# Kernel tuning notes

Measured on AMD Instinct MI355X. Metric: run time of the kernel, lower is better.

## Reference

```python
import jax, jax.numpy as jnp
import numpy as np

B, S, H, D = 2, 2048, 16, 64
DM = H * D  # 1024


def setup_inputs() -> dict:
    key = jax.random.key(0)
    ks = jax.random.split(key, 5)
    scale = 0.02
    return {
        "hidden_states": jax.random.normal(ks[0], (B, S, DM), dtype=jnp.float32),
        "Wq": scale * jax.random.normal(ks[1], (DM, DM), dtype=jnp.float32),
        "bq": jnp.zeros((DM,), jnp.float32),
        "Wk": scale * jax.random.normal(ks[2], (DM, DM), dtype=jnp.float32),
        "bk": jnp.zeros((DM,), jnp.float32),
        "Wv": scale * jax.random.normal(ks[3], (DM, DM), dtype=jnp.float32),
        "bv": jnp.zeros((DM,), jnp.float32),
        "Wy": scale * jax.random.normal(ks[4], (DM, DM), dtype=jnp.float32),
        "by": jnp.zeros((DM,), jnp.float32),
    }


def _split_heads(x):
    # [B,S,H*D] -> [B,H,S,D]
    b, s, _ = x.shape
    return x.reshape(b, s, H, D).transpose(0, 2, 1, 3)


def _merge_heads(x):
    # [B,H,S,D] -> [B,S,H*D]
    b, h, s, d = x.shape
    return x.transpose(0, 2, 1, 3).reshape(b, s, h * d)


def reference(hidden_states, Wq, bq, Wk, bk, Wv, bv, Wy, by):
    q = _split_heads(hidden_states @ Wq.T + bq)  # [B,H,S,D]
    k = _split_heads(hidden_states @ Wk.T + bk)
    v = _split_heads(hidden_states @ Wv.T + bv)

    logits = jnp.einsum("bhsd,bhtd->bhst", q, k) / jnp.sqrt(jnp.float32(D))
    mask = jnp.tril(jnp.ones((S, S), jnp.float32))  # causal lower-triangular mask

    # Faithful to the original module's hand-rolled masked softmax:
    # denominator = sum_t exp(logits) * mask ; numerator = exp(logits*mask - 1e4*(1-mask))
    denom = jnp.sum(jnp.exp(logits) * mask, axis=3, keepdims=True)
    numer = jnp.exp(logits * mask - 1e4 * (1.0 - mask))
    weights = numer / denom  # [B,H,S,S]

    attended = jnp.einsum("bhst,bhtd->bhsd", weights, v)
    out = _merge_heads(attended)  # [B,S,H*D]
    return out @ Wy.T + by
```

## Files before the change

### kernel.cpp

```cpp
#include <hip/hip_runtime.h>

#define DEV __device__ __forceinline__

typedef __attribute__((ext_vector_type(8))) short bf16x8;
typedef __attribute__((ext_vector_type(4))) float f32x4;
typedef __attribute__((ext_vector_type(16))) float f32x16;

DEV ushort f2bf(float f) {
  union { float f; unsigned u; } x; x.f = f;
  unsigned r = (x.u + 0x7FFFu + ((x.u >> 16) & 1u)) >> 16;
  return (ushort)r;
}

DEV void gload16(const void* g, void* l) {
  __builtin_amdgcn_global_load_lds(
      (const __attribute__((address_space(1))) void*)g,
      (__attribute__((address_space(3))) void*)l, 16, 0, 0);
}

DEV f32x4 mfma16(bf16x8 a, bf16x8 b, f32x4 c) {
  return __builtin_amdgcn_mfma_f32_16x16x32_bf16(a, b, c, 0, 0, 0);
}
DEV f32x16 mfma32(bf16x8 a, bf16x8 b, f32x16 c) {
  return __builtin_amdgcn_mfma_f32_32x32x16_bf16(a, b, c, 0, 0, 0);
}

DEV unsigned cvtpk(float a, float b) {
  unsigned r;
  asm("v_cvt_pk_bf16_f32 %0, %1, %2" : "=v"(r) : "v"(a), "v"(b));
  return r;
}

#if __has_builtin(__builtin_amdgcn_exp2f)
#define EXP2(x) __builtin_amdgcn_exp2f(x)
#else
#define EXP2(x) exp2f(x)
#endif

#define BB 2
#define SS 2048
#define HH 16
#define DD 64
#define DM 1024
#define MROWS (BB * SS)
#define NQKV  (3 * DM)

__global__ void convert_kernel(const float* __restrict__ hs,
                               const float* __restrict__ Wq, const float* __restrict__ bq,
                               const float* __restrict__ Wk, const float* __restrict__ bk,
                               const float* __restrict__ Wv, const float* __restrict__ bv,
                               const float* __restrict__ Wy,
                               ushort* __restrict__ Xb, ushort* __restrict__ Wqkv,
                               ushort* __restrict__ Wyb, float* __restrict__ bqkv) {
  const int HS_V = (MROWS * DM) / 4;
  const int WQ_V = (NQKV * DM) / 4;
  const int WY_V = (DM * DM) / 4;
  int idx = blockIdx.x * 256 + threadIdx.x;
  if (idx < HS_V) {
    float4 v = ((const float4*)hs)[idx];
    ushort4 o; o.x = f2bf(v.x); o.y = f2bf(v.y); o.z = f2bf(v.z); o.w = f2bf(v.w);
    ((ushort4*)Xb)[idx] = o;
  } else if (idx < HS_V + WQ_V) {
    int e = (idx - HS_V) * 4;
    int n = e >> 10, k = e & 1023;
    const float* W = (n < 1024) ? Wq : (n < 2048) ? Wk : Wv;
    int nn = n & 1023;
    float4 v = *(const float4*)(W + nn * 1024 + k);
    ushort4 o; o.x = f2bf(v.x); o.y = f2bf(v.y); o.z = f2bf(v.z); o.w = f2bf(v.w);
    ((ushort4*)Wqkv)[idx - HS_V] = o;
  } else if (idx < HS_V + WQ_V + WY_V) {
    int e = idx - HS_V - WQ_V;
    float4 v = ((const float4*)Wy)[e];
    ushort4 o; o.x = f2bf(v.x); o.y = f2bf(v.y); o.z = f2bf(v.z); o.w = f2bf(v.w);
    ((ushort4*)Wyb)[e] = o;
  }
  if (idx < NQKV)
    bqkv[idx] = (idx < 1024) ? bq[idx] : (idx < 2048) ? bk[idx - 1024] : bv[idx - 2048];
}

template <int MI, bool OUT_F32>
__global__ void gemm_bt(const ushort* __restrict__ A, const ushort* __restrict__ Bw,
                        const float* __restrict__ bias, void* __restrict__ Cout,
                        int M, int N, int K, int scaleN, float qscale) {
  constexpr int BM = 64 * MI;
  constexpr int NI = BM / 32;
  __shared__ ushort Al[BM * 64];
  __shared__ ushort Bl[128 * 64];
  const int tid = threadIdx.x;
  const int lane = tid & 63;
  const int wave = tid >> 6;
  const int lg = lane >> 4, l15 = lane & 15;
  const int m0 = blockIdx.x * BM, n0 = blockIdx.y * 128;
  const int wm = (wave >> 1) * (BM / 2), wn = (wave & 1) * 64;

  f32x4 acc[NI][4] = {};

  for (int k0 = 0; k0 < K; k0 += 64) {
#pragma unroll
    for (int s = 0; s < BM * 8 / 256; ++s) {
      int f = tid + s * 256;
      int row = f >> 3, c = f & 7, cs = c ^ (row & 7);
      gload16(A + (size_t)(m0 + row) * K + k0 + cs * 8, (char*)Al + f * 16);
    }
#pragma unroll
    for (int s = 0; s < 4; ++s) {
      int f = tid + s * 256;
      int row = f >> 3, c = f & 7, cs = c ^ (row & 7);
      gload16(Bw + (size_t)(n0 + row) * K + k0 + cs * 8, (char*)Bl + f * 16);
    }
    __syncthreads();

#pragma unroll
    for (int kk = 0; kk < 2; ++kk) {
      bf16x8 af[NI], bfr[4];
#pragma unroll
      for (int i = 0; i < NI; ++i) {
        int rA = wm + i * 16 + l15;
        int cA = (kk * 4 + lg) ^ (rA & 7);
        af[i] = *(const bf16x8*)((const char*)Al + rA * 128 + cA * 16);
      }
#pragma unroll
      for (int j = 0; j < 4; ++j) {
        int rB = wn + j * 16 + l15;
        int cB = (kk * 4 + lg) ^ (rB & 7);
        bfr[j] = *(const bf16x8*)((const char*)Bl + rB * 128 + cB * 16);
      }
#pragma unroll
      for (int i = 0; i < NI; ++i)
#pragma unroll
        for (int j = 0; j < 4; ++j)
          acc[i][j] = mfma16(af[i], bfr[j], acc[i][j]);
    }
    __syncthreads();
  }

#pragma unroll
  for (int i = 0; i < NI; ++i) {
#pragma unroll
    for (int j = 0; j < 4; ++j) {
      int n = n0 + wn + j * 16 + l15;
      float bv = bias[n];
      float qs = (n < scaleN) ? qscale : 1.0f;
#pragma unroll
      for (int r = 0; r < 4; ++r) {
        int m = m0 + wm + i * 16 + lg * 4 + r;
        float v = (acc[i][j][r] + bv) * qs;
        if (OUT_F32)
          ((float*)Cout)[(size_t)m * N + n] = v;
        else
          ((ushort*)Cout)[(size_t)m * N + n] = f2bf(v);
      }
    }
  }
}

__global__ void transpose_v(const ushort* __restrict__ QKV, ushort* __restrict__ Vt) {
  __shared__ ushort tl[64][72];
  const int tid = threadIdx.x;
  const int bh = blockIdx.y, b = bh >> 4, h = bh & 15;
  const int s0 = blockIdx.x * 64;
  {
    int s = tid >> 2, d0 = (tid & 3) * 16;
    const ushort* src = QKV + (size_t)(b * SS + s0 + s) * NQKV + 2 * DM + h * DD + d0;
    bf16x8 v0 = *(const bf16x8*)(src);
    bf16x8 v1 = *(const bf16x8*)(src + 8);
#pragma unroll
    for (int i = 0; i < 8; ++i) tl[d0 + i][s] = (ushort)v0[i];
#pragma unroll
    for (int i = 0; i < 8; ++i) tl[d0 + 8 + i][s] = (ushort)v1[i];
  }
  __syncthreads();
  {
    int d = tid >> 2, s1 = (tid & 3) * 16;
    ushort* dst = Vt + (size_t)(bh * DD + d) * SS + s0 + s1;
    *(bf16x8*)(dst) = *(const bf16x8*)&tl[d][s1];
    *(bf16x8*)(dst + 8) = *(const bf16x8*)&tl[d][s1 + 8];
  }
}

__global__ __launch_bounds__(256, 2)
void attn_kernel(const ushort* __restrict__ QKV, const ushort* __restrict__ Vt,
                 ushort* __restrict__ Ob) {
  __shared__ __align__(16) char SMEM[65536];

  const int tid = threadIdx.x;
  const int wave = tid >> 6, lane = tid & 63;
  const int l31 = lane & 31, hi = lane >> 5;
  const int grp = wave >> 1, wq = wave & 1;

  const int n = blockIdx.x;
  const int bh = (n & 7) | ((n >> 7) << 3);
  const int pairi = (n >> 3) & 15;
  const int b = bh >> 4, h = bh & 15;

  int px = lane, pw = 1000;
  asm volatile("v_permlane32_swap_b32 %0, %1" : "+v"(px), "+v"(pw));
  const bool defA = (__builtin_amdgcn_readfirstlane(px) == 0);

  const int gtid = tid & 127;
  const int srow = gtid >> 3;
  const int scs = (gtid & 7) ^ (srow & 7);
  const ushort* Kg = QKV + (size_t)(b * SS + srow) * NQKV + DM + h * 64 + scs * 8;
  const ushort* Vg = Vt + (size_t)(bh * 64 + srow) * SS + scs * 8;

#define STAGE(d_, kv0_) do {                                            \
    const ushort* kg_ = Kg + (size_t)(kv0_) * NQKV;                     \
    const ushort* vg_ = Vg + (kv0_);                                    \
    char* kl_ = SMEM + (grp * 2 + (d_)) * 8192 + gtid * 16;             \
    char* vl_ = SMEM + 32768 + (grp * 2 + (d_)) * 8192 + gtid * 16;     \
    _Pragma("unroll")                                                   \
    for (int s_ = 0; s_ < 4; ++s_) {                                    \
      gload16(kg_ + (size_t)s_ * 16 * NQKV, kl_ + s_ * 2048);           \
      gload16(vg_ + (size_t)s_ * 16 * SS,   vl_ + s_ * 2048);           \
    }                                                                   \
  } while (0)

  union U4 { unsigned u[4]; bf16x8 v; };

#define PACKH(sv, R, D0, D1, D2, D3) do {                              \
    unsigned X = cvtpk(sv[R + 0], sv[R + 1]);                          \
    unsigned Y = cvtpk(sv[R + 2], sv[R + 3]);                          \
    unsigned W = cvtpk(sv[R + 4], sv[R + 5]);                          \
    unsigned Z = cvtpk(sv[R + 6], sv[R + 7]);                          \
    if (defA) {                                                        \
      asm volatile("v_permlane32_swap_b32 %0, %1" : "+v"(X), "+v"(W)); \
      asm volatile("v_permlane32_swap_b32 %0, %1" : "+v"(Y), "+v"(Z)); \
    } else {                                                           \
      asm volatile("v_permlane32_swap_b32 %0, %1" : "+v"(W), "+v"(X)); \
      asm volatile("v_permlane32_swap_b32 %0, %1" : "+v"(Z), "+v"(Y)); \
    }                                                                  \
    D0 = X; D1 = Y; D2 = W; D3 = Z;                                    \
  } while (0)

#pragma unroll 1
  for (int ph = 0; ph < 2; ++ph) {
    __builtin_amdgcn_s_barrier();

    const int qt = ph ? (31 - pairi) : pairi;
    const int q0 = qt * 64;
    const int nkv = qt + 1;
    const int niter = (nkv + 1) >> 1;
    const int qw = q0 + wq * 32;
    const int q_lane = qw + l31;

    const ushort* Qrow = QKV + (size_t)(b * SS + q_lane) * NQKV + h * 64 + hi * 8;
    bf16x8 qf0 = *(const bf16x8*)(Qrow);
    bf16x8 qf1 = *(const bf16x8*)(Qrow + 16);
    bf16x8 qf2 = *(const bf16x8*)(Qrow + 32);
    bf16x8 qf3 = *(const bf16x8*)(Qrow + 48);

    f32x16 acc0 = {}, acc1 = {};
    float ps0 = 0.f, ps1 = 0.f, ps2 = 0.f, ps3 = 0.f;

    if (grp < nkv) STAGE(0, grp * 64);
    int buf = 0;

#pragma unroll 1
    for (int it = 0; it < niter; ++it) {
      const int j = 2 * it + grp;
      if (j + 2 < nkv) {
        STAGE(buf ^ 1, (j + 2) * 64);
        asm volatile("s_waitcnt vmcnt(8)" ::: "memory");
      } else {
        asm volatile("s_waitcnt vmcnt(0)" ::: "memory");
      }
      __builtin_amdgcn_s_barrier();
      __builtin_amdgcn_sched_barrier(0);

      if (j < nkv) {
        const int kv0 = j * 64;
        const char* Kb = SMEM + (grp * 2 + buf) * 8192;
        const char* Vb = SMEM + 32768 + (grp * 2 + buf) * 8192;

        f32x16 s0 = {}, s1 = {};
        __builtin_amdgcn_s_setprio(1);
#pragma unroll
        for (int ks = 0; ks < 4; ++ks) {
          const int ch = (((ks * 2 + hi) ^ (l31 & 7)) * 16);
          bf16x8 kfa = *(const bf16x8*)(Kb + l31 * 128 + ch);
          bf16x8 kfb = *(const bf16x8*)(Kb + (l31 + 32) * 128 + ch);
          bf16x8 qk = (ks == 0) ? qf0 : (ks == 1) ? qf1 : (ks == 2) ? qf2 : qf3;
          s0 = mfma32(kfa, qk, s0);
          s1 = mfma32(kfb, qk, s1);
        }
        __builtin_amdgcn_s_setprio(0);

        if (j == qt) {
#pragma unroll
          for (int r = 0; r < 16; ++r) {
            const int tb = (r & 3) + 8 * (r >> 2) + 4 * hi;
            if (kv0 + tb > q_lane) s0[r] = -1e30f;
            if (kv0 + 32 + tb > q_lane) s1[r] = -1e30f;
          }
        }

#pragma unroll
        for (int r = 0; r < 16; r += 4) {
          float a0 = EXP2(s0[r]), a1 = EXP2(s0[r + 1]), a2 = EXP2(s0[r + 2]), a3 = EXP2(s0[r + 3]);
          s0[r] = a0; s0[r + 1] = a1; s0[r + 2] = a2; s0[r + 3] = a3;
          ps0 += a0; ps1 += a1; ps2 += a2; ps3 += a3;
          float b0 = EXP2(s1[r]), b1 = EXP2(s1[r + 1]), b2 = EXP2(s1[r + 2]), b3 = EXP2(s1[r + 3]);
          s1[r] = b0; s1[r + 1] = b1; s1[r + 2] = b2; s1[r + 3] = b3;
          ps0 += b0; ps1 += b1; ps2 += b2; ps3 += b3;
        }

        U4 f0, f1, f2, f3;
        PACKH(s0, 0, f0.u[0], f0.u[1], f0.u[2], f0.u[3]);
        PACKH(s0, 8, f1.u[0], f1.u[1], f1.u[2], f1.u[3]);
        PACKH(s1, 0, f2.u[0], f2.u[1], f2.u[2], f2.u[3]);
        PACKH(s1, 8, f3.u[0], f3.u[1], f3.u[2], f3.u[3]);

        __builtin_amdgcn_s_setprio(1);
#pragma unroll
        for (int ts = 0; ts < 4; ++ts) {
          const int ch = (((ts * 2 + hi) ^ (l31 & 7)) * 16);
          bf16x8 vfa = *(const bf16x8*)(Vb + l31 * 128 + ch);
          bf16x8 vfb = *(const bf16x8*)(Vb + (l31 + 32) * 128 + ch);
          bf16x8 pf = (ts == 0) ? f0.v : (ts == 1) ? f1.v : (ts == 2) ? f2.v : f3.v;
          acc0 = mfma32(vfa, pf, acc0);
          acc1 = mfma32(vfb, pf, acc1);
        }
        __builtin_amdgcn_s_setprio(0);
      }
      __builtin_amdgcn_sched_barrier(0);
      __builtin_amdgcn_s_barrier();
      buf ^= 1;
    }

    float psum = ps0 + ps1 + ps2 + ps3;
    f32x4* MA = (f32x4*)SMEM;
    float* MP = (float*)(SMEM + 32768);
    const int slot = wq * 64 + lane;
    if (grp == 1) {
#pragma unroll
      for (int c = 0; c < 4; ++c) {
        f32x4 t0 = {acc0[4 * c], acc0[4 * c + 1], acc0[4 * c + 2], acc0[4 * c + 3]};
        MA[c * 128 + slot] = t0;
        f32x4 t1 = {acc1[4 * c], acc1[4 * c + 1], acc1[4 * c + 2], acc1[4 * c + 3]};
        MA[(c + 4) * 128 + slot] = t1;
      }
      MP[slot] = psum;
    }
    __builtin_amdgcn_s_barrier();
    if (grp == 0) {
#pragma unroll
      for (int c = 0; c < 4; ++c) {
        f32x4 t0 = MA[c * 128 + slot];
        f32x4 t1 = MA[(c + 4) * 128 + slot];
        acc0[4 * c] += t0[0]; acc0[4 * c + 1] += t0[1];
        acc0[4 * c + 2] += t0[2]; acc0[4 * c + 3] += t0[3];
        acc1[4 * c] += t1[0]; acc1[4 * c + 1] += t1[1];
        acc1[4 * c + 2] += t1[2]; acc1[4 * c + 3] += t1[3];
      }
      psum += MP[slot];
      float tot = psum + __shfl_xor(psum, 32, 64);
      float inv = 1.0f / tot;
      ushort* orow = Ob + (size_t)(b * SS + q_lane) * DM + h * 64;
#pragma unroll
      for (int g = 0; g < 4; ++g) {
        uint2 st;
        st.x = cvtpk(acc0[4 * g + 0] * inv, acc0[4 * g + 1] * inv);
        st.y = cvtpk(acc0[4 * g + 2] * inv, acc0[4 * g + 3] * inv);
        *(uint2*)(orow + 8 * g + 4 * hi) = st;
        uint2 st2;
        st2.x = cvtpk(acc1[4 * g + 0] * inv, acc1[4 * g + 1] * inv);
        st2.y = cvtpk(acc1[4 * g + 2] * inv, acc1[4 * g + 3] * inv);
        *(uint2*)(orow + 32 + 8 * g + 4 * hi) = st2;
      }
    }
  }
#undef STAGE
#undef PACKH
}

extern "C" void kernel_launch(void* const* d_in, const int* in_sizes, int n_in,
                              void* d_out, int out_size, void* d_ws, size_t ws_size,
                              hipStream_t stream) {
  const float* hs = (const float*)d_in[0];
  const float* Wq = (const float*)d_in[1];
  const float* bq = (const float*)d_in[2];
  const float* Wk = (const float*)d_in[3];
  const float* bk = (const float*)d_in[4];
  const float* Wv = (const float*)d_in[5];
  const float* bv = (const float*)d_in[6];
  const float* Wy = (const float*)d_in[7];
  const float* by = (const float*)d_in[8];
  float* out = (float*)d_out;

  char* ws = (char*)d_ws;
  ushort* Xb   = (ushort*)(ws);
  ushort* Wqkv = (ushort*)(ws + (8ull  << 20));
  ushort* Wyb  = (ushort*)(ws + (14ull << 20));
  float*  bqkv = (float*) (ws + (16ull << 20));
  ushort* QKV  = (ushort*)(ws + (17ull << 20));
  ushort* Vt   = (ushort*)(ws + (41ull << 20));
  ushort* Ob   = (ushort*)(ws + (49ull << 20));

  const float QSC = 0.125f * 1.44269504088896f;

  convert_kernel<<<dim3(8192), dim3(256), 0, stream>>>(hs, Wq, bq, Wk, bk, Wv, bv, Wy,
                                                       Xb, Wqkv, Wyb, bqkv);
  gemm_bt<2, false><<<dim3(32, 24), dim3(256), 0, stream>>>(Xb, Wqkv, bqkv, QKV,
                                                            MROWS, NQKV, DM, 1024, QSC);
  transpose_v<<<dim3(32, 32), dim3(256), 0, stream>>>(QKV, Vt);
  attn_kernel<<<dim3(512), dim3(256), 0, stream>>>(QKV, Vt, Ob);
  gemm_bt<1, true><<<dim3(64, 8), dim3(256), 0, stream>>>(Ob, Wyb, by, out,
                                                          MROWS, DM, DM, 0, 1.0f);
}
```

Baseline: 93.20 us.

## Double-buffer GEMM k-loop with register prefetch and fuse V transpose into QKV epilogue

The GEMM main loop now uses two LDS slots: it prefetches the k-tile two steps ahead through direct-to-LDS loads and loads the next tile's fragments into registers while MFMAs run. This replaces the single-buffered load, sync, compute sequence. The QKV projection epilogue writes the V columns directly in transposed [b,h,d,s] layout, which removes the separate transpose_v kernel and the V section of the QKV buffer. The cost is more LDS per block and hand-tuned waitcnt and barrier placement, and the transposed V stores are 8-byte scattered writes.

```diff
diff --git a/kernel.cpp b/kernel.cpp
--- a/kernel.cpp
+++ b/kernel.cpp
@@ -44,6 +44,7 @@
 #define DM 1024
 #define MROWS (BB * SS)
 #define NQKV  (3 * DM)
+#define NQK   (2 * DM)
 
 __global__ void convert_kernel(const float* __restrict__ hs,
                                const float* __restrict__ Wq, const float* __restrict__ bq,
@@ -78,14 +79,17 @@
     bqkv[idx] = (idx < 1024) ? bq[idx] : (idx < 2048) ? bk[idx - 1024] : bv[idx - 2048];
 }
 
-template <int MI, bool OUT_F32>
+template <int BM, bool OUT_F32, bool VSPLIT>
 __global__ void gemm_bt(const ushort* __restrict__ A, const ushort* __restrict__ Bw,
                         const float* __restrict__ bias, void* __restrict__ Cout,
-                        int M, int N, int K, int scaleN, float qscale) {
-  constexpr int BM = 64 * MI;
+                        ushort* __restrict__ VtOut,
+                        int M, int N, int K, int Nc, int scaleN, float qscale) {
   constexpr int NI = BM / 32;
-  __shared__ ushort Al[BM * 64];
-  __shared__ ushort Bl[128 * 64];
+  constexpr int ASTEPS = BM / 32;
+  constexpr int LOADS = ASTEPS + 4;
+  constexpr int SLOT = (BM + 128) * 128;
+  __shared__ __align__(16) char GL[2 * SLOT];
+
   const int tid = threadIdx.x;
   const int lane = tid & 63;
   const int wave = tid >> 6;
@@ -94,92 +98,130 @@
   const int wm = (wave >> 1) * (BM / 2), wn = (wave & 1) * 64;
 
   f32x4 acc[NI][4] = {};
-
-  for (int k0 = 0; k0 < K; k0 += 64) {
-#pragma unroll
-    for (int s = 0; s < BM * 8 / 256; ++s) {
-      int f = tid + s * 256;
-      int row = f >> 3, c = f & 7, cs = c ^ (row & 7);
-      gload16(A + (size_t)(m0 + row) * K + k0 + cs * 8, (char*)Al + f * 16);
-    }
-#pragma unroll
-    for (int s = 0; s < 4; ++s) {
-      int f = tid + s * 256;
-      int row = f >> 3, c = f & 7, cs = c ^ (row & 7);
-      gload16(Bw + (size_t)(n0 + row) * K + k0 + cs * 8, (char*)Bl + f * 16);
-    }
-    __syncthreads();
-
-#pragma unroll
-    for (int kk = 0; kk < 2; ++kk) {
-      bf16x8 af[NI], bfr[4];
-#pragma unroll
-      for (int i = 0; i < NI; ++i) {
-        int rA = wm + i * 16 + l15;
-        int cA = (kk * 4 + lg) ^ (rA & 7);
-        af[i] = *(const bf16x8*)((const char*)Al + rA * 128 + cA * 16);
-      }
+  bf16x8 af[NI][2], bfr[4][2];
+
+  const int srow = tid >> 3;
+  const int scs = (tid & 7) ^ (srow & 7);
+
+#define STAGE(p_, k0_) do {                                              \
+    _Pragma("unroll")                                                    \
+    for (int s_ = 0; s_ < ASTEPS; ++s_)                                  \
+      gload16(A + (size_t)(m0 + srow + s_ * 32) * K + (k0_) + scs * 8,   \
+              GL + (p_) * SLOT + (tid + s_ * 256) * 16);                 \
+    _Pragma("unroll")                                                    \
+    for (int s_ = 0; s_ < 4; ++s_)                                       \
+      gload16(Bw + (size_t)(n0 + srow + s_ * 32) * K + (k0_) + scs * 8,  \
+              GL + (p_) * SLOT + BM * 128 + (tid + s_ * 256) * 16);      \
+  } while (0)
+
+#define LOADFRAGS(p_) do {                                               \
+    const char* Ab_ = GL + (p_) * SLOT;                                  \
+    const char* Bb_ = Ab_ + BM * 128;                                    \
+    _Pragma("unroll")                                                    \
+    for (int kk_ = 0; kk_ < 2; ++kk_) {                                  \
+      _Pragma("unroll")                                                  \
+      for (int i_ = 0; i_ < NI; ++i_) {                                  \
+        int rA_ = wm + i_ * 16 + l15;                                    \
+        int cA_ = (kk_ * 4 + lg) ^ (rA_ & 7);                            \
+        af[i_][kk_] = *(const bf16x8*)(Ab_ + rA_ * 128 + cA_ * 16);      \
+      }                                                                  \
+      _Pragma("unroll")                                                  \
+      for (int j_ = 0; j_ < 4; ++j_) {                                   \
+        int rB_ = wn + j_ * 16 + l15;                                    \
+        int cB_ = (kk_ * 4 + lg) ^ (rB_ & 7);                            \
+        bfr[j_][kk_] = *(const bf16x8*)(Bb_ + rB_ * 128 + cB_ * 16);     \
+      }                                                                  \
+    }                                                                    \
+  } while (0)
+
+#define VMCNT_L() do {                                                   \
+    if constexpr (LOADS == 8) asm volatile("s_waitcnt vmcnt(8)" ::: "memory"); \
+    else asm volatile("s_waitcnt vmcnt(6)" ::: "memory");                \
+  } while (0)
+#define VMCNT_0() asm volatile("s_waitcnt vmcnt(0)" ::: "memory")
+
+  const int nt = K >> 6;
+  int p = 0;
+
+  STAGE(0, 0);
+  if (nt > 1) { STAGE(1, 64); VMCNT_L(); } else { VMCNT_0(); }
+  __builtin_amdgcn_s_barrier();
+  __builtin_amdgcn_sched_barrier(0);
+  LOADFRAGS(0);
+  asm volatile("s_waitcnt lgkmcnt(0)" ::: "memory");
+  __builtin_amdgcn_sched_barrier(0);
+
+#pragma unroll 1
+  for (int t = 0; t < nt; ++t) {
+    __builtin_amdgcn_s_barrier();
+    __builtin_amdgcn_sched_barrier(0);
+    const bool pre = (t + 2 < nt);
+    if (pre) STAGE(p, (t + 2) << 6);
+#pragma unroll
+    for (int kk = 0; kk < 2; ++kk)
+#pragma unroll
+      for (int i = 0; i < NI; ++i)
+#pragma unroll
+        for (int j = 0; j < 4; ++j)
+          acc[i][j] = mfma16(af[i][kk], bfr[j][kk], acc[i][j]);
+    if (pre) VMCNT_L();
+    else VMCNT_0();
+    __builtin_amdgcn_s_barrier();
+    __builtin_amdgcn_sched_barrier(0);
+    if (t + 1 < nt) {
+      LOADFRAGS(p ^ 1);
+      asm volatile("s_waitcnt lgkmcnt(0)" ::: "memory");
+      __builtin_amdgcn_sched_barrier(0);
+    }
+    p ^= 1;
+  }
+
+  if (VSPLIT && n0 >= 2048) {
+#pragma unroll
+    for (int i = 0; i < NI; ++i) {
 #pragma unroll
       for (int j = 0; j < 4; ++j) {
-        int rB = wn + j * 16 + l15;
-        int cB = (kk * 4 + lg) ^ (rB & 7);
-        bfr[j] = *(const bf16x8*)((const char*)Bl + rB * 128 + cB * 16);
-      }
-#pragma unroll
-      for (int i = 0; i < NI; ++i)
-#pragma unroll
-        for (int j = 0; j < 4; ++j)
-          acc[i][j] = mfma16(af[i], bfr[j], acc[i][j]);
-    }
-    __syncthreads();
+        int n = n0 + wn + j * 16 + l15;
+        float bv = bias[n];
+        int h = (n >> 6) & 15, d = n & 63;
+        int mb = m0 + wm + i * 16 + lg * 4;
+        int b = mb >> 11, s = mb & 2047;
+        ushort4 o;
+        o.x = f2bf(acc[i][j][0] + bv);
+        o.y = f2bf(acc[i][j][1] + bv);
+        o.z = f2bf(acc[i][j][2] + bv);
+        o.w = f2bf(acc[i][j][3] + bv);
+        *(ushort4*)(VtOut + ((size_t)(b * 16 + h) * 64 + d) * SS + s) = o;
+      }
+    }
+  } else {
+#pragma unroll
+    for (int i = 0; i < NI; ++i) {
+#pragma unroll
+      for (int j = 0; j < 4; ++j) {
+        int n = n0 + wn + j * 16 + l15;
+        float bv = bias[n];
+        float qs = (n < scaleN) ? qscale : 1.0f;
+#pragma unroll
+        for (int r = 0; r < 4; ++r) {
+          int m = m0 + wm + i * 16 + lg * 4 + r;
+          float v = (acc[i][j][r] + bv) * qs;
+          if (OUT_F32)
+            ((float*)Cout)[(size_t)m * Nc + n] = v;
+          else
+            ((ushort*)Cout)[(size_t)m * Nc + n] = f2bf(v);
+        }
+      }
+    }
   }
-
-#pragma unroll
-  for (int i = 0; i < NI; ++i) {
-#pragma unroll
-    for (int j = 0; j < 4; ++j) {
-      int n = n0 + wn + j * 16 + l15;
-      float bv = bias[n];
-      float qs = (n < scaleN) ? qscale : 1.0f;
-#pragma unroll
-      for (int r = 0; r < 4; ++r) {
-        int m = m0 + wm + i * 16 + lg * 4 + r;
-        float v = (acc[i][j][r] + bv) * qs;
-        if (OUT_F32)
-          ((float*)Cout)[(size_t)m * N + n] = v;
-        else
-          ((ushort*)Cout)[(size_t)m * N + n] = f2bf(v);
-      }
-    }
-  }
-}
-
-__global__ void transpose_v(const ushort* __restrict__ QKV, ushort* __restrict__ Vt) {
-  __shared__ ushort tl[64][72];
-  const int tid = threadIdx.x;
-  const int bh = blockIdx.y, b = bh >> 4, h = bh & 15;
-  const int s0 = blockIdx.x * 64;
-  {
-    int s = tid >> 2, d0 = (tid & 3) * 16;
-    const ushort* src = QKV + (size_t)(b * SS + s0 + s) * NQKV + 2 * DM + h * DD + d0;
-    bf16x8 v0 = *(const bf16x8*)(src);
-    bf16x8 v1 = *(const bf16x8*)(src + 8);
-#pragma unroll
-    for (int i = 0; i < 8; ++i) tl[d0 + i][s] = (ushort)v0[i];
-#pragma unroll
-    for (int i = 0; i < 8; ++i) tl[d0 + 8 + i][s] = (ushort)v1[i];
-  }
-  __syncthreads();
-  {
-    int d = tid >> 2, s1 = (tid & 3) * 16;
-    ushort* dst = Vt + (size_t)(bh * DD + d) * SS + s0 + s1;
-    *(bf16x8*)(dst) = *(const bf16x8*)&tl[d][s1];
-    *(bf16x8*)(dst + 8) = *(const bf16x8*)&tl[d][s1 + 8];
-  }
+#undef STAGE
+#undef LOADFRAGS
+#undef VMCNT_L
+#undef VMCNT_0
 }
 
 __global__ __launch_bounds__(256, 2)
-void attn_kernel(const ushort* __restrict__ QKV, const ushort* __restrict__ Vt,
+void attn_kernel(const ushort* __restrict__ QK, const ushort* __restrict__ Vt,
                  ushort* __restrict__ Ob) {
   __shared__ __align__(16) char SMEM[65536];
 
@@ -200,18 +242,18 @@
   const int gtid = tid & 127;
   const int srow = gtid >> 3;
   const int scs = (gtid & 7) ^ (srow & 7);
-  const ushort* Kg = QKV + (size_t)(b * SS + srow) * NQKV + DM + h * 64 + scs * 8;
+  const ushort* Kg = QK + (size_t)(b * SS + srow) * NQK + DM + h * 64 + scs * 8;
   const ushort* Vg = Vt + (size_t)(bh * 64 + srow) * SS + scs * 8;
 
 #define STAGE(d_, kv0_) do {                                            \
-    const ushort* kg_ = Kg + (size_t)(kv0_) * NQKV;                     \
+    const ushort* kg_ = Kg + (size_t)(kv0_) * NQK;                      \
     const ushort* vg_ = Vg + (kv0_);                                    \
     char* kl_ = SMEM + (grp * 2 + (d_)) * 8192 + gtid * 16;             \
     char* vl_ = SMEM + 32768 + (grp * 2 + (d_)) * 8192 + gtid * 16;     \
     _Pragma("unroll")                                                   \
     for (int s_ = 0; s_ < 4; ++s_) {                                    \
-      gload16(kg_ + (size_t)s_ * 16 * NQKV, kl_ + s_ * 2048);           \
-      gload16(vg_ + (size_t)s_ * 16 * SS,   vl_ + s_ * 2048);           \
+      gload16(kg_ + (size_t)s_ * 16 * NQK, kl_ + s_ * 2048);            \
+      gload16(vg_ + (size_t)s_ * 16 * SS,  vl_ + s_ * 2048);            \
     }                                                                   \
   } while (0)
 
@@ -243,7 +285,7 @@
     const int qw = q0 + wq * 32;
     const int q_lane = qw + l31;
 
-    const ushort* Qrow = QKV + (size_t)(b * SS + q_lane) * NQKV + h * 64 + hi * 8;
+    const ushort* Qrow = QK + (size_t)(b * SS + q_lane) * NQK + h * 64 + hi * 8;
     bf16x8 qf0 = *(const bf16x8*)(Qrow);
     bf16x8 qf1 = *(const bf16x8*)(Qrow + 16);
     bf16x8 qf2 = *(const bf16x8*)(Qrow + 32);
@@ -392,18 +434,17 @@
   ushort* Wqkv = (ushort*)(ws + (8ull  << 20));
   ushort* Wyb  = (ushort*)(ws + (14ull << 20));
   float*  bqkv = (float*) (ws + (16ull << 20));
-  ushort* QKV  = (ushort*)(ws + (17ull << 20));
-  ushort* Vt   = (ushort*)(ws + (41ull << 20));
-  ushort* Ob   = (ushort*)(ws + (49ull << 20));
+  ushort* QK   = (ushort*)(ws + (17ull << 20));
+  ushort* Vt   = (ushort*)(ws + (33ull << 20));
+  ushort* Ob   = (ushort*)(ws + (41ull << 20));
 
   const float QSC = 0.125f * 1.44269504088896f;
 
   convert_kernel<<<dim3(8192), dim3(256), 0, stream>>>(hs, Wq, bq, Wk, bk, Wv, bv, Wy,
                                                        Xb, Wqkv, Wyb, bqkv);
-  gemm_bt<2, false><<<dim3(32, 24), dim3(256), 0, stream>>>(Xb, Wqkv, bqkv, QKV,
-                                                            MROWS, NQKV, DM, 1024, QSC);
-  transpose_v<<<dim3(32, 32), dim3(256), 0, stream>>>(QKV, Vt);
-  attn_kernel<<<dim3(512), dim3(256), 0, stream>>>(QKV, Vt, Ob);
-  gemm_bt<1, true><<<dim3(64, 8), dim3(256), 0, stream>>>(Ob, Wyb, by, out,
-                                                          MROWS, DM, DM, 0, 1.0f);
-}
+  gemm_bt<128, false, true><<<dim3(32, 24), dim3(256), 0, stream>>>(
+      Xb, Wqkv, bqkv, QK, Vt, MROWS, NQKV, DM, NQK, 1024, QSC);
+  attn_kernel<<<dim3(512), dim3(256), 0, stream>>>(QK, Vt, Ob);
+  gemm_bt<64, true, false><<<dim3(64, 8), dim3(256), 0, stream>>>(
+      Ob, Wyb, by, out, nullptr, MROWS, DM, DM, DM, 0, 1.0f);
+}
```

New measurement: 182.3 us. 1.96x slower.

## Fuse V transpose into QKV GEMM epilogue, drop transpose kernel

Applied to the files above, without the earlier changes.

The QKV projection GEMM now writes V directly in transposed [b,h,d,s] layout from its epilogue, and Q/K go to a narrower QK buffer with row stride 2*DM. This removes the separate transpose_v kernel launch along with its read and write of the V tensor. The trade-off is that the epilogue's V stores are 8-byte ushort4 writes strided across rows, which coalesce less well than the plain row-major stores.

```diff
diff --git a/kernel.cpp b/kernel.cpp
--- a/kernel.cpp
+++ b/kernel.cpp
@@ -44,6 +44,7 @@
 #define DM 1024
 #define MROWS (BB * SS)
 #define NQKV  (3 * DM)
+#define NQK   (2 * DM)
 
 __global__ void convert_kernel(const float* __restrict__ hs,
                                const float* __restrict__ Wq, const float* __restrict__ bq,
@@ -78,11 +79,11 @@
     bqkv[idx] = (idx < 1024) ? bq[idx] : (idx < 2048) ? bk[idx - 1024] : bv[idx - 2048];
 }
 
-template <int MI, bool OUT_F32>
+template <int BM, bool OUT_F32, bool VSPLIT>
 __global__ void gemm_bt(const ushort* __restrict__ A, const ushort* __restrict__ Bw,
                         const float* __restrict__ bias, void* __restrict__ Cout,
-                        int M, int N, int K, int scaleN, float qscale) {
-  constexpr int BM = 64 * MI;
+                        ushort* __restrict__ VtOut,
+                        int M, int N, int K, int Nc, int scaleN, float qscale) {
   constexpr int NI = BM / 32;
   __shared__ ushort Al[BM * 64];
   __shared__ ushort Bl[128 * 64];
@@ -134,52 +135,48 @@
     __syncthreads();
   }
 
-#pragma unroll
-  for (int i = 0; i < NI; ++i) {
-#pragma unroll
-    for (int j = 0; j < 4; ++j) {
-      int n = n0 + wn + j * 16 + l15;
-      float bv = bias[n];
-      float qs = (n < scaleN) ? qscale : 1.0f;
-#pragma unroll
-      for (int r = 0; r < 4; ++r) {
-        int m = m0 + wm + i * 16 + lg * 4 + r;
-        float v = (acc[i][j][r] + bv) * qs;
-        if (OUT_F32)
-          ((float*)Cout)[(size_t)m * N + n] = v;
-        else
-          ((ushort*)Cout)[(size_t)m * N + n] = f2bf(v);
+  if (VSPLIT && n0 >= 2048) {
+#pragma unroll
+    for (int i = 0; i < NI; ++i) {
+#pragma unroll
+      for (int j = 0; j < 4; ++j) {
+        int n = n0 + wn + j * 16 + l15;
+        float bv = bias[n];
+        int h = (n >> 6) & 15, d = n & 63;
+        int mb = m0 + wm + i * 16 + lg * 4;
+        int b = mb >> 11, s = mb & 2047;
+        ushort4 o;
+        o.x = f2bf(acc[i][j][0] + bv);
+        o.y = f2bf(acc[i][j][1] + bv);
+        o.z = f2bf(acc[i][j][2] + bv);
+        o.w = f2bf(acc[i][j][3] + bv);
+        *(ushort4*)(VtOut + ((size_t)(b * 16 + h) * 64 + d) * SS + s) = o;
+      }
+    }
+  } else {
+#pragma unroll
+    for (int i = 0; i < NI; ++i) {
+#pragma unroll
+      for (int j = 0; j < 4; ++j) {
+        int n = n0 + wn + j * 16 + l15;
+        float bv = bias[n];
+        float qs = (n < scaleN) ? qscale : 1.0f;
+#pragma unroll
+        for (int r = 0; r < 4; ++r) {
+          int m = m0 + wm + i * 16 + lg * 4 + r;
+          float v = (acc[i][j][r] + bv) * qs;
+          if (OUT_F32)
+            ((float*)Cout)[(size_t)m * Nc + n] = v;
+          else
+            ((ushort*)Cout)[(size_t)m * Nc + n] = f2bf(v);
+        }
       }
     }
   }
 }
 
-__global__ void transpose_v(const ushort* __restrict__ QKV, ushort* __restrict__ Vt) {
-  __shared__ ushort tl[64][72];
-  const int tid = threadIdx.x;
-  const int bh = blockIdx.y, b = bh >> 4, h = bh & 15;
-  const int s0 = blockIdx.x * 64;
-  {
-    int s = tid >> 2, d0 = (tid & 3) * 16;
-    const ushort* src = QKV + (size_t)(b * SS + s0 + s) * NQKV + 2 * DM + h * DD + d0;
-    bf16x8 v0 = *(const bf16x8*)(src);
-    bf16x8 v1 = *(const bf16x8*)(src + 8);
-#pragma unroll
-    for (int i = 0; i < 8; ++i) tl[d0 + i][s] = (ushort)v0[i];
-#pragma unroll
-    for (int i = 0; i < 8; ++i) tl[d0 + 8 + i][s] = (ushort)v1[i];
-  }
-  __syncthreads();
-  {
-    int d = tid >> 2, s1 = (tid & 3) * 16;
-    ushort* dst = Vt + (size_t)(bh * DD + d) * SS + s0 + s1;
-    *(bf16x8*)(dst) = *(const bf16x8*)&tl[d][s1];
-    *(bf16x8*)(dst + 8) = *(const bf16x8*)&tl[d][s1 + 8];
-  }
-}
-
 __global__ __launch_bounds__(256, 2)
-void attn_kernel(const ushort* __restrict__ QKV, const ushort* __restrict__ Vt,
+void attn_kernel(const ushort* __restrict__ QK, const ushort* __restrict__ Vt,
                  ushort* __restrict__ Ob) {
   __shared__ __align__(16) char SMEM[65536];
 
@@ -200,18 +197,18 @@
   const int gtid = tid & 127;
   const int srow = gtid >> 3;
   const int scs = (gtid & 7) ^ (srow & 7);
-  const ushort* Kg = QKV + (size_t)(b * SS + srow) * NQKV + DM + h * 64 + scs * 8;
+  const ushort* Kg = QK + (size_t)(b * SS + srow) * NQK + DM + h * 64 + scs * 8;
   const ushort* Vg = Vt + (size_t)(bh * 64 + srow) * SS + scs * 8;
 
 #define STAGE(d_, kv0_) do {                                            \
-    const ushort* kg_ = Kg + (size_t)(kv0_) * NQKV;                     \
+    const ushort* kg_ = Kg + (size_t)(kv0_) * NQK;                      \
     const ushort* vg_ = Vg + (kv0_);                                    \
     char* kl_ = SMEM + (grp * 2 + (d_)) * 8192 + gtid * 16;             \
     char* vl_ = SMEM + 32768 + (grp * 2 + (d_)) * 8192 + gtid * 16;     \
     _Pragma("unroll")                                                   \
     for (int s_ = 0; s_ < 4; ++s_) {                                    \
-      gload16(kg_ + (size_t)s_ * 16 * NQKV, kl_ + s_ * 2048);           \
-      gload16(vg_ + (size_t)s_ * 16 * SS,   vl_ + s_ * 2048);           \
+      gload16(kg_ + (size_t)s_ * 16 * NQK, kl_ + s_ * 2048);            \
+      gload16(vg_ + (size_t)s_ * 16 * SS,  vl_ + s_ * 2048);            \
     }                                                                   \
   } while (0)
 
@@ -243,7 +240,7 @@
     const int qw = q0 + wq * 32;
     const int q_lane = qw + l31;
 
-    const ushort* Qrow = QKV + (size_t)(b * SS + q_lane) * NQKV + h * 64 + hi * 8;
+    const ushort* Qrow = QK + (size_t)(b * SS + q_lane) * NQK + h * 64 + hi * 8;
     bf16x8 qf0 = *(const bf16x8*)(Qrow);
     bf16x8 qf1 = *(const bf16x8*)(Qrow + 16);
     bf16x8 qf2 = *(const bf16x8*)(Qrow + 32);
@@ -392,18 +389,17 @@
   ushort* Wqkv = (ushort*)(ws + (8ull  << 20));
   ushort* Wyb  = (ushort*)(ws + (14ull << 20));
   float*  bqkv = (float*) (ws + (16ull << 20));
-  ushort* QKV  = (ushort*)(ws + (17ull << 20));
-  ushort* Vt   = (ushort*)(ws + (41ull << 20));
-  ushort* Ob   = (ushort*)(ws + (49ull << 20));
+  ushort* QK   = (ushort*)(ws + (17ull << 20));
+  ushort* Vt   = (ushort*)(ws + (33ull << 20));
+  ushort* Ob   = (ushort*)(ws + (41ull << 20));
 
   const float QSC = 0.125f * 1.44269504088896f;
 
   convert_kernel<<<dim3(8192), dim3(256), 0, stream>>>(hs, Wq, bq, Wk, bk, Wv, bv, Wy,
                                                        Xb, Wqkv, Wyb, bqkv);
-  gemm_bt<2, false><<<dim3(32, 24), dim3(256), 0, stream>>>(Xb, Wqkv, bqkv, QKV,
-                                                            MROWS, NQKV, DM, 1024, QSC);
-  transpose_v<<<dim3(32, 32), dim3(256), 0, stream>>>(QKV, Vt);
-  attn_kernel<<<dim3(512), dim3(256), 0, stream>>>(QKV, Vt, Ob);
-  gemm_bt<1, true><<<dim3(64, 8), dim3(256), 0, stream>>>(Ob, Wyb, by, out,
-                                                          MROWS, DM, DM, 0, 1.0f);
-}
+  gemm_bt<128, false, true><<<dim3(32, 24), dim3(256), 0, stream>>>(
+      Xb, Wqkv, bqkv, QK, Vt, MROWS, NQKV, DM, NQK, 1024, QSC);
+  attn_kernel<<<dim3(512), dim3(256), 0, stream>>>(QK, Vt, Ob);
+  gemm_bt<64, true, false><<<dim3(64, 8), dim3(256), 0, stream>>>(
+      Ob, Wyb, by, out, nullptr, MROWS, DM, DM, DM, 0, 1.0f);
+}
```

Measured after the change: 88.82 us (median of 5 runs). -4.7%, faster.
